# Optimization experiments

Hardware: AMD Instinct MI355X
Metric: run time of the kernel (lower is better)

Reference implementation:

```python
import jax, jax.numpy as jnp
import numpy as np

B, HEADS, N, D, K2 = 8, 8, 3136, 32, 9

def setup_inputs() -> dict:
    key = jax.random.key(0)
    k1, k2, k3, k4, k5 = jax.random.split(key, 5)
    return {
        "q_norm": jax.random.normal(k1, (B, HEADS, N, D), dtype=jnp.float32),
        "attn_local": jax.random.normal(k2, (B, HEADS, N, K2), dtype=jnp.float32),
        "v_local": jax.random.normal(k3, (B, HEADS, N, D, K2), dtype=jnp.float32),
        "learnable_tokens": jax.random.normal(k4, (HEADS, D, K2), dtype=jnp.float32),
        "learnable_bias": jax.random.normal(k5, (HEADS, N, K2), dtype=jnp.float32),
        "window_size": 3,
        "H": 56,
        "W": 56,
    }

def reference(q_norm, attn_local, v_local, learnable_tokens, learnable_bias, window_size, H, W):
    # attn = q_norm @ learnable_tokens + learnable_bias + attn_local  -> [B,h,N,k^2]
    attn = jnp.einsum('bhnd,hdk->bhnk', q_norm, learnable_tokens) + learnable_bias + attn_local
    # out = attn @ v_local^T over the window axis -> [B,h,N,d]
    return jnp.einsum('bhnk,bhndk->bhnd', attn, v_local)
```

## Files before the change

kernel.cpp:

```cpp
#include <hip/hip_runtime.h>

constexpr int Bc   = 8;
constexpr int Hh   = 8;
constexpr int Nn   = 3136;
constexpr int Dd   = 32;
constexpr int K2c  = 9;
constexpr int ROWS = Bc * Hh * Nn;
constexpr int ROWS_PER_BLOCK = 8;
constexpr int BLOCK = 256;

__global__ __launch_bounds__(BLOCK, 4)
void swattn_av_kernel(const float* __restrict__ q,
                      const float* __restrict__ attn_local,
                      const float* __restrict__ v,
                      const float* __restrict__ tok,
                      const float* __restrict__ bias,
                      float* __restrict__ out) {
    __shared__ float T_lds[Dd * K2c];
    __shared__ float q_lds[ROWS_PER_BLOCK][Dd + 1];
    __shared__ float attn_lds[ROWS_PER_BLOCK][K2c];

    const int tid  = threadIdx.x;
    const int base = blockIdx.x * ROWS_PER_BLOCK;
    const int h    = (base / Nn) % Hh;

    T_lds[tid < Dd * K2c ? tid : 0] = tok[h * Dd * K2c + (tid < Dd * K2c ? tid : 0)];
    if (tid < Dd * K2c - BLOCK)
        T_lds[BLOCK + tid] = tok[h * Dd * K2c + BLOCK + tid];
    {
        const int lrow = tid >> 5, d = tid & 31;
        q_lds[lrow][d] = q[(base + lrow) * Dd + d];
    }
    __syncthreads();

    if (tid < ROWS_PER_BLOCK * K2c) {
        const int lrow = tid / K2c;
        const int k    = tid - lrow * K2c;
        const int gr   = base + lrow;
        float s0 = 0.f, s1 = 0.f, s2 = 0.f, s3 = 0.f;
        #pragma unroll
        for (int d = 0; d < Dd; d += 4) {
            s0 += q_lds[lrow][d + 0] * T_lds[(d + 0) * K2c + k];
            s1 += q_lds[lrow][d + 1] * T_lds[(d + 1) * K2c + k];
            s2 += q_lds[lrow][d + 2] * T_lds[(d + 2) * K2c + k];
            s3 += q_lds[lrow][d + 3] * T_lds[(d + 3) * K2c + k];
        }
        const int bn = gr % (Hh * Nn);
        attn_lds[lrow][k] = ((s0 + s1) + (s2 + s3))
                          + attn_local[gr * K2c + k]
                          + bias[bn * K2c + k];
    }
    __syncthreads();

    {
        const int lrow = tid >> 5, d = tid & 31;
        const int gr   = base + lrow;
        const float* __restrict__ vr = v + (size_t)gr * (Dd * K2c) + d * K2c;
        float acc = 0.f;
        #pragma unroll
        for (int k = 0; k < K2c; ++k)
            acc += attn_lds[lrow][k] * vr[k];
        out[gr * Dd + d] = acc;
    }
}

extern "C" void kernel_launch(void* const* d_in, const int* in_sizes, int n_in,
                              void* d_out, int out_size, void* d_ws, size_t ws_size,
                              hipStream_t stream) {
    const float* q          = (const float*)d_in[0];
    const float* attn_local = (const float*)d_in[1];
    const float* v          = (const float*)d_in[2];
    const float* tok        = (const float*)d_in[3];
    const float* bias       = (const float*)d_in[4];
    float* out = (float*)d_out;

    const int grid = ROWS / ROWS_PER_BLOCK;
    swattn_av_kernel<<<grid, BLOCK, 0, stream>>>(q, attn_local, v, tok, bias, out);
}
```

Baseline: 345.2 us.

## Stage v tile in LDS with coalesced float4 loads and hoist attn/bias loads

The block's whole v slab (8 rows × 288 floats) is now copied into shared memory with coalesced float4 loads before the first barrier, so the final reduction reads v from LDS instead of making stride-9 global reads per thread. q and token loads become float4, and attn_local/bias loads move ahead of the barrier so their latency overlaps the other loads. This adds about 9KB of LDS per block, which may limit occupancy, and the strided LDS reads of v may cause bank conflicts.

```diff
diff --git a/kernel.cpp b/kernel.cpp
--- a/kernel.cpp
+++ b/kernel.cpp
@@ -6,8 +6,9 @@
 constexpr int Dd   = 32;
 constexpr int K2c  = 9;
 constexpr int ROWS = Bc * Hh * Nn;
-constexpr int ROWS_PER_BLOCK = 8;
+constexpr int RPB  = 8;
 constexpr int BLOCK = 256;
+constexpr int VT4  = RPB * Dd * K2c / 4;
 
 __global__ __launch_bounds__(BLOCK, 4)
 void swattn_av_kernel(const float* __restrict__ q,
@@ -16,27 +17,42 @@
                       const float* __restrict__ tok,
                       const float* __restrict__ bias,
                       float* __restrict__ out) {
-    __shared__ float T_lds[Dd * K2c];
-    __shared__ float q_lds[ROWS_PER_BLOCK][Dd + 1];
-    __shared__ float attn_lds[ROWS_PER_BLOCK][K2c];
+    __shared__ float4 v_lds4[VT4];
+    __shared__ float  T_lds[Dd * K2c] __attribute__((aligned(16)));
+    __shared__ float  q_lds[RPB][Dd + 1];
+    __shared__ float  attn_lds[RPB][K2c];
 
     const int tid  = threadIdx.x;
-    const int base = blockIdx.x * ROWS_PER_BLOCK;
+    const int base = blockIdx.x * RPB;
     const int h    = (base / Nn) % Hh;
 
-    T_lds[tid < Dd * K2c ? tid : 0] = tok[h * Dd * K2c + (tid < Dd * K2c ? tid : 0)];
-    if (tid < Dd * K2c - BLOCK)
-        T_lds[BLOCK + tid] = tok[h * Dd * K2c + BLOCK + tid];
     {
-        const int lrow = tid >> 5, d = tid & 31;
-        q_lds[lrow][d] = q[(base + lrow) * Dd + d];
+        const float4* __restrict__ vsrc = (const float4*)(v + (size_t)base * (Dd * K2c));
+        v_lds4[tid]       = vsrc[tid];
+        v_lds4[tid + 256] = vsrc[tid + 256];
+        if (tid < VT4 - 512) v_lds4[tid + 512] = vsrc[tid + 512];
+    }
+    if (tid < RPB * Dd / 4) {
+        const int lrow = tid >> 3, dg = tid & 7;
+        const float4 qv = ((const float4*)(q + (size_t)(base + lrow) * Dd))[dg];
+        q_lds[lrow][dg * 4 + 0] = qv.x;
+        q_lds[lrow][dg * 4 + 1] = qv.y;
+        q_lds[lrow][dg * 4 + 2] = qv.z;
+        q_lds[lrow][dg * 4 + 3] = qv.w;
+    }
+    if (tid < Dd * K2c / 4)
+        ((float4*)T_lds)[tid] = ((const float4*)(tok + (size_t)h * Dd * K2c))[tid];
+
+    float al = 0.f, bi = 0.f;
+    if (tid < RPB * K2c) {
+        al = attn_local[(size_t)base * K2c + tid];
+        bi = bias[(size_t)(base % (Hh * Nn)) * K2c + tid];
     }
     __syncthreads();
 
-    if (tid < ROWS_PER_BLOCK * K2c) {
+    if (tid < RPB * K2c) {
         const int lrow = tid / K2c;
         const int k    = tid - lrow * K2c;
-        const int gr   = base + lrow;
         float s0 = 0.f, s1 = 0.f, s2 = 0.f, s3 = 0.f;
         #pragma unroll
         for (int d = 0; d < Dd; d += 4) {
@@ -45,22 +61,19 @@
             s2 += q_lds[lrow][d + 2] * T_lds[(d + 2) * K2c + k];
             s3 += q_lds[lrow][d + 3] * T_lds[(d + 3) * K2c + k];
         }
-        const int bn = gr % (Hh * Nn);
-        attn_lds[lrow][k] = ((s0 + s1) + (s2 + s3))
-                          + attn_local[gr * K2c + k]
-                          + bias[bn * K2c + k];
+        attn_lds[lrow][k] = ((s0 + s1) + (s2 + s3)) + al + bi;
     }
     __syncthreads();
 
     {
         const int lrow = tid >> 5, d = tid & 31;
-        const int gr   = base + lrow;
-        const float* __restrict__ vr = v + (size_t)gr * (Dd * K2c) + d * K2c;
+        const float* __restrict__ vr =
+            (const float*)v_lds4 + lrow * (Dd * K2c) + d * K2c;
         float acc = 0.f;
         #pragma unroll
         for (int k = 0; k < K2c; ++k)
             acc += attn_lds[lrow][k] * vr[k];
-        out[gr * Dd + d] = acc;
+        out[(size_t)base * Dd + tid] = acc;
     }
 }
 
@@ -74,6 +87,6 @@
     const float* bias       = (const float*)d_in[4];
     float* out = (float*)d_out;
 
-    const int grid = ROWS / ROWS_PER_BLOCK;
+    const int grid = ROWS / RPB;
     swattn_av_kernel<<<grid, BLOCK, 0, stream>>>(q, attn_local, v, tok, bias, out);
 }
```

New measurement: 347.1 us. About the same (+0.5%).
